# Optimization experiments

Measured on AMD Instinct MI355X. Metric: run time of the kernel, lower is better.

Reference implementation:

```python
import jax, jax.numpy as jnp
import numpy as np

B, C_IN, C_MID, C_OUT, H, W = 256, 2, 128, 64, 15, 15
N_RES = 4  # line_length//2 - 1 with line_length=11

# per-direction input offsets for kernel taps w0 and w2 (w1 is always center),
# matching fix_direction_order=True sparse 3x3 kernel construction:
# dir0 horizontal, dir1 vertical, dir2 anti-diagonal, dir3 main diagonal.
OFFSETS = (((0, -1), (0, 1)),
           ((-1, 0), (1, 0)),
           ((1, -1), (-1, 1)),
           ((-1, -1), (1, 1)))


def shift2d(x, di, dj):
    # out[..., i, j] = x[..., i+di, j+dj] with zero padding (di,dj in {-1,0,1})
    nd = x.ndim
    xp = jnp.pad(x, [(0, 0)] * (nd - 2) + [(1, 1), (1, 1)])
    h, w = x.shape[-2], x.shape[-1]
    return xp[..., 1 + di:1 + di + h, 1 + dj:1 + dj + w]


def dir_conv(x, w, b):
    # x: [4,B,Cin,H,W]; w: [Cout,Cin,3]; b: [Cout]
    x0 = jnp.stack([shift2d(x[d], *OFFSETS[d][0]) for d in range(4)])
    x2 = jnp.stack([shift2d(x[d], *OFFSETS[d][1]) for d in range(4)])
    y = (jnp.einsum('oc,dbchw->dbohw', w[..., 0], x0)
         + jnp.einsum('oc,dbchw->dbohw', w[..., 1], x)
         + jnp.einsum('oc,dbchw->dbohw', w[..., 2], x2))
    return y + b[None, None, :, None, None]


def conv1x1(x, w, b):
    # x: [4,B,Cin,H,W]; w: [Cout,Cin]; b: [Cout]
    return jnp.einsum('oc,dbchw->dbohw', w, x) + b[None, None, :, None, None]


def setup_inputs() -> dict:
    key = jax.random.key(0)
    ks = jax.random.split(key, 16)
    s_in = 1.0 / np.sqrt(3 * C_IN)
    s_mid = 1.0 / np.sqrt(3 * C_MID)
    s_pw = 1.0 / np.sqrt(C_MID)
    return {
        'x': jax.random.normal(ks[0], (B, C_IN, H, W), jnp.float32),
        'dconv0_w': jax.random.normal(ks[1], (C_MID, C_IN, 3), jnp.float32) * s_in,
        'dconv0_b': jnp.zeros((C_MID,), jnp.float32),
        'res_dconv_w': jax.random.normal(ks[2], (N_RES, C_MID, C_MID, 3), jnp.float32) * s_mid,
        'res_dconv_b': jnp.zeros((N_RES, C_MID), jnp.float32),
        'res_pw_w': jax.random.normal(ks[3], (N_RES, C_MID, C_MID), jnp.float32) * s_pw,
        'res_pw_b': jnp.zeros((N_RES, C_MID), jnp.float32),
        'c0_w1': jax.random.normal(ks[4], (C_MID, C_MID), jnp.float32) * s_pw,
        'c0_b1': jnp.zeros((C_MID,), jnp.float32),
        'c0_w2': jax.random.normal(ks[5], (C_MID, C_MID), jnp.float32) * s_pw,
        'c0_b2': jnp.zeros((C_MID,), jnp.float32),
        'final_w': jax.random.normal(ks[6], (C_OUT, C_MID), jnp.float32) * s_pw,
        'final_b': jnp.zeros((C_OUT,), jnp.float32),
    }


def reference(x, dconv0_w, dconv0_b, res_dconv_w, res_dconv_b,
              res_pw_w, res_pw_b, c0_w1, c0_b1, c0_w2, c0_b2,
              final_w, final_b):
    act = jax.nn.silu
    # all 4 direction streams start from the same input plane
    h = jnp.broadcast_to(x[None], (4,) + x.shape)  # [4,B,Cin,H,W]
    h = act(dir_conv(h, dconv0_w, dconv0_b))
    # DirectionalConvResBlocks (norm='none')
    for i in range(N_RES):
        r = h
        h = act(dir_conv(h, res_dconv_w[i], res_dconv_b[i]))
        h = act(conv1x1(h, res_pw_w[i], res_pw_b[i]))
        h = h + r
    # Conv0dResBlock (two 1x1 convs, middle_dim_multipler=1)
    r = h
    h = act(conv1x1(h, c0_w1, c0_b1))
    h = act(conv1x1(h, c0_w2, c0_b2))
    h = h + r
    # final 1x1 conv, then stack directions at dim=1 -> [B,4,Cout,H,W]
    h = conv1x1(h, final_w, final_b)
    return jnp.transpose(h, (1, 0, 2, 3, 4))
```

## Files before the change

### kernel.cpp

```cpp
#include <hip/hip_runtime.h>

using u16 = unsigned short;
using u32 = unsigned int;

typedef __bf16 bf16x8 __attribute__((ext_vector_type(8)));
typedef float  f32x4  __attribute__((ext_vector_type(4)));

#define NPOS   225
#define NT     15
#define ROWP   136
#define A_ROWS 289
#define B_ROWS 241
#define A_ELEMS (A_ROWS*ROWP)
#define B_ELEMS (B_ROWS*ROWP)
#define LDS_BYTES ((A_ELEMS + B_ELEMS)*2)
#define RSTRIDE17 (17*ROWP)

#define WA_PER_L 49152
#define WP_OFF   (4*WA_PER_L)
#define WP_PER   16384
#define WF_OFF   (WP_OFF + 6*WP_PER)
#define W_U16_TOTAL (WF_OFF + 8192)

__host__ __device__ __forceinline__ int permc(int c){
  return (c & ~0x3C) | (((c >> 2) & 3) << 4) | (((c >> 4) & 3) << 2);
}

__device__ __forceinline__ float bflo(u32 q){ return __uint_as_float(q << 16); }
__device__ __forceinline__ float bfhi(u32 q){ return __uint_as_float(q & 0xffff0000u); }
__device__ __forceinline__ u16 f2bf(float f){
  u32 u = __float_as_uint(f);
  return (u16)((u + 0x7fffu + ((u >> 16) & 1u)) >> 16);
}
__device__ __forceinline__ u32 packbf(float a, float b){
  union { __bf16 h[2]; u32 u; } r;
  r.h[0] = (__bf16)a; r.h[1] = (__bf16)b;
  return r.u;
}
__device__ __forceinline__ float silu_f(float x){
  return x * __builtin_amdgcn_rcpf(1.f + __expf(-x));
}
__device__ __forceinline__ f32x4 mfma16(bf16x8 a, bf16x8 b, f32x4 c){
  return __builtin_amdgcn_mfma_f32_16x16x32_bf16(a, b, c, 0, 0, 0);
}

__global__ void prep_w(const float* __restrict__ d0w, const float* __restrict__ d0b,
                       const float* __restrict__ rdw,
                       const float* __restrict__ rpw, const float* __restrict__ c1w,
                       const float* __restrict__ c2w, const float* __restrict__ fw,
                       float* __restrict__ ws)
{
  u16* wsb = (u16*)(ws + 896);
  const int total = 896 + W_U16_TOTAL;
  for (int idx = blockIdx.x*blockDim.x + threadIdx.x; idx < total; idx += gridDim.x*blockDim.x){
    if (idx < 768){
      int k = idx >> 7, s = idx & 127;
      ws[idx] = d0w[permc(s)*6 + k];
      continue;
    }
    if (idx < 896){
      int s = idx - 768;
      ws[idx] = d0b[permc(s)];
      continue;
    }
    int e = idx - 896;
    float v;
    if (e < WP_OFF){
      int L = e / WA_PER_L, r = e % WA_PER_L;
      int og = r / 24576; int r1 = r - og*24576;
      int tap = r1 >> 13; int r2 = r1 & 8191;
      int ot = r2 >> 11, kb = (r2 >> 9) & 3, l = (r2 >> 3) & 63, j = r2 & 7;
      int o = (og*4 + ot)*16 + (l & 15);
      int ks = kb*32 + ((l >> 4) << 3) + j;
      v = rdw[((L*128 + o)*128 + permc(ks))*3 + tap];
    } else if (e < WF_OFF){
      int t2 = e - WP_OFF;
      int i = t2 / WP_PER, r = t2 % WP_PER;
      int og2 = r >> 13;
      int ot = (r >> 11) & 3, kb = (r >> 9) & 3, l = (r >> 3) & 63, j = r & 7;
      int o = (og2*4 + ot)*16 + (l & 15);
      int ks = kb*32 + ((l >> 4) << 3) + j;
      v = (i < 4) ? rpw[(i*128 + o)*128 + permc(ks)]
        : (i == 4) ? c1w[o*128 + permc(ks)] : c2w[o*128 + permc(ks)];
    } else {
      int e2 = e - WF_OFF;
      int ot = e2 >> 11, kb = (e2 >> 9) & 3, l = (e2 >> 3) & 63, j = e2 & 7;
      int o = ot*16 + (l & 15);
      int ks = kb*32 + ((l >> 4) << 3) + j;
      v = fw[o*128 + permc(ks)];
    }
    wsb[e] = f2bf(v);
  }
}

__device__ __forceinline__ uint4 pack_silu2(const f32x4& a, const f32x4& b){
  uint4 q;
  q.x = packbf(silu_f(a[0]), silu_f(a[1]));
  q.y = packbf(silu_f(a[2]), silu_f(a[3]));
  q.z = packbf(silu_f(b[0]), silu_f(b[1]));
  q.w = packbf(silu_f(b[2]), silu_f(b[3]));
  return q;
}

template<int NTL>
__device__ __forceinline__ void dconv_mfma(const u16* __restrict__ As, u16* __restrict__ Bs,
    const u16* __restrict__ wloc, const float* __restrict__ bias,
    int lane, int og, int T0, int off0, int off2)
{
  const int col = lane & 15, kg = lane >> 4, koff = kg*8;
  f32x4 acc[4][NTL];
  #pragma unroll
  for (int ot=0; ot<4; ++ot){
    f32x4 bz = *(const f32x4*)(bias + og*64 + ot*16 + kg*4);
    #pragma unroll
    for (int t=0;t<NTL;++t) acc[ot][t] = bz;
  }
  const int c1 = (col+1)*ROWP + koff;
  #pragma unroll 1
  for (int tap=0; tap<3; ++tap){
    const int offr = (tap==0) ? off0 : (tap==1) ? 0 : off2;
    bf16x8 w[4][4];
    #pragma unroll
    for (int ot=0; ot<4; ++ot)
      #pragma unroll
      for (int kb=0; kb<4; ++kb)
        w[ot][kb] = *(const bf16x8*)(wloc + tap*8192 + ot*2048 + kb*512 + lane*8);
    #pragma unroll
    for (int t=0; t<NTL; ++t){
      const u16* s = As + (T0+t+1)*RSTRIDE17 + c1 + offr;
      __builtin_amdgcn_s_setprio(1);
      #pragma unroll
      for (int kb=0; kb<4; ++kb){
        bf16x8 v = *(const bf16x8*)(s + kb*32);
        acc[0][t] = mfma16(w[0][kb], v, acc[0][t]);
        acc[1][t] = mfma16(w[1][kb], v, acc[1][t]);
        acc[2][t] = mfma16(w[2][kb], v, acc[2][t]);
        acc[3][t] = mfma16(w[3][kb], v, acc[3][t]);
      }
      __builtin_amdgcn_s_setprio(0);
    }
  }
  if (col < 15){
    #pragma unroll
    for (int t=0;t<NTL;++t){
      u16* dp = Bs + ((T0+t)*16+col)*ROWP + og*64 + kg*16;
      uint4 q0 = pack_silu2(acc[0][t], acc[1][t]);
      uint4 q1 = pack_silu2(acc[2][t], acc[3][t]);
      *(uint4*)dp = q0;
      *(uint4*)(dp+8) = q1;
    }
  }
}

template<bool SRC_HALO, bool DST_HALO, bool RESID>
__device__ __forceinline__ void pw_mfma(const u16* __restrict__ src, u16* __restrict__ dst,
    const u16* __restrict__ wloc, const float* __restrict__ bias,
    int lane, int og2, int T0, int T1)
{
  const int col = lane & 15, kg = lane >> 4, koff = kg*8;
  bf16x8 wp[4][4];
  #pragma unroll
  for (int ot=0; ot<4; ++ot)
    #pragma unroll
    for (int kb=0; kb<4; ++kb)
      wp[ot][kb] = *(const bf16x8*)(wloc + og2*8192 + ot*2048 + kb*512 + lane*8);
  f32x4 bz[4];
  #pragma unroll
  for (int ot=0; ot<4; ++ot) bz[ot] = *(const f32x4*)(bias + og2*64 + ot*16 + kg*4);
  const int c1 = (col+1)*ROWP;
  #pragma unroll 2
  for (int tile=T0; tile<T1; ++tile){
    const int rh = (tile+1)*RSTRIDE17 + c1;
    const int rc = (tile*16+col)*ROWP;
    const u16* S = src + (SRC_HALO ? rh : rc) + koff;
    f32x4 a0 = bz[0], a1 = bz[1], a2 = bz[2], a3 = bz[3];
    __builtin_amdgcn_s_setprio(1);
    #pragma unroll
    for (int kb=0; kb<4; ++kb){
      bf16x8 v = *(const bf16x8*)(S + kb*32);
      a0 = mfma16(wp[0][kb], v, a0);
      a1 = mfma16(wp[1][kb], v, a1);
      a2 = mfma16(wp[2][kb], v, a2);
      a3 = mfma16(wp[3][kb], v, a3);
    }
    __builtin_amdgcn_s_setprio(0);
    if (col < 15){
      u16* dp = dst + (DST_HALO ? rh : rc) + og2*64 + kg*16;
      float s0 = silu_f(a0[0]), s1 = silu_f(a0[1]), s2 = silu_f(a0[2]), s3 = silu_f(a0[3]);
      float s4 = silu_f(a1[0]), s5 = silu_f(a1[1]), s6 = silu_f(a1[2]), s7 = silu_f(a1[3]);
      float s8 = silu_f(a2[0]), s9 = silu_f(a2[1]), sa = silu_f(a2[2]), sb = silu_f(a2[3]);
      float sc = silu_f(a3[0]), sd = silu_f(a3[1]), se = silu_f(a3[2]), sf = silu_f(a3[3]);
      if (RESID){
        uint4 r0 = *(const uint4*)dp;
        uint4 r1 = *(const uint4*)(dp+8);
        s0 += bflo(r0.x); s1 += bfhi(r0.x); s2 += bflo(r0.y); s3 += bfhi(r0.y);
        s4 += bflo(r0.z); s5 += bfhi(r0.z); s6 += bflo(r0.w); s7 += bfhi(r0.w);
        s8 += bflo(r1.x); s9 += bfhi(r1.x); sa += bflo(r1.y); sb += bfhi(r1.y);
        sc += bflo(r1.z); sd += bfhi(r1.z); se += bflo(r1.w); sf += bfhi(r1.w);
      }
      uint4 q0, q1;
      q0.x = packbf(s0, s1); q0.y = packbf(s2, s3);
      q0.z = packbf(s4, s5); q0.w = packbf(s6, s7);
      q1.x = packbf(s8, s9); q1.y = packbf(sa, sb);
      q1.z = packbf(sc, sd); q1.w = packbf(se, sf);
      *(uint4*)dp = q0;
      *(uint4*)(dp+8) = q1;
    }
  }
}

__device__ __forceinline__ void fin_mfma(const u16* __restrict__ As,
    const u16* __restrict__ wloc, const float* __restrict__ bias,
    float* __restrict__ out, int lane, int ogf, int T0, int T1, int bd)
{
  const int col = lane & 15, kg = lane >> 4, koff = kg*8;
  bf16x8 wf[2][4];
  #pragma unroll
  for (int ot=0; ot<2; ++ot)
    #pragma unroll
    for (int kb=0; kb<4; ++kb)
      wf[ot][kb] = *(const bf16x8*)(wloc + (ogf*2+ot)*2048 + kb*512 + lane*8);
  f32x4 bz0 = *(const f32x4*)(bias + ogf*32 + kg*4);
  f32x4 bz1 = *(const f32x4*)(bias + ogf*32 + 16 + kg*4);
  const int c1 = (col+1)*ROWP;
  #pragma unroll 1
  for (int tile=T0; tile<T1; ++tile){
    const u16* S = As + (tile+1)*RSTRIDE17 + c1 + koff;
    f32x4 a0 = bz0, a1 = bz1;
    __builtin_amdgcn_s_setprio(1);
    #pragma unroll
    for (int kb=0; kb<4; ++kb){
      bf16x8 v = *(const bf16x8*)(S + kb*32);
      a0 = mfma16(wf[0][kb], v, a0);
      a1 = mfma16(wf[1][kb], v, a1);
    }
    __builtin_amdgcn_s_setprio(0);
    if (col < 15){
      float* op = out + ((size_t)(bd*64 + ogf*32 + kg*4))*NPOS + tile*15 + col;
      op[0]      = a0[0];
      op[NPOS]   = a0[1];
      op[2*NPOS] = a0[2];
      op[3*NPOS] = a0[3];
      float* oq = op + 16*NPOS;
      oq[0]      = a1[0];
      oq[NPOS]   = a1[1];
      oq[2*NPOS] = a1[2];
      oq[3*NPOS] = a1[3];
    }
  }
}

__global__ void __launch_bounds__(512, 2)
mix9_main(const float* __restrict__ x,
          const float* __restrict__ b_rd,
          const float* __restrict__ b_rp,
          const float* __restrict__ b_c1,
          const float* __restrict__ b_c2,
          const float* __restrict__ b_fin,
          const float* __restrict__ wt,
          float* __restrict__ out)
{
  extern __shared__ u16 sm[];
  u16* As = sm;
  u16* Bs = sm + A_ELEMS;

  const int blk  = blockIdx.x;
  const int b    = blk >> 2, d = blk & 3;
  const int tid  = threadIdx.x;
  const int wave = __builtin_amdgcn_readfirstlane(tid >> 6);
  const int lane = tid & 63;

  const int ogd  = wave >> 2;
  const int pgd  = wave & 3;
  const int og2  = wave >> 2;
  const int ph4  = wave & 3;
  const int T0p  = ph4 * 4;
  const int T1p  = (ph4 == 3) ? NT : T0p + 4;
  const int ob   = wave * 16;

  const int DI0[4] = {0,-1, 1,-1}, DJ0[4] = {-1, 0,-1,-1};
  const int DI2[4] = {0, 1,-1, 1}, DJ2[4] = { 1, 0, 1, 1};
  const int di0 = DI0[d], dj0 = DJ0[d], di2 = DI2[d], dj2 = DJ2[d];
  const int off0 = (di0*17 + dj0)*ROWP;
  const int off2 = (di2*17 + dj2)*ROWP;

  for (int k2 = tid; k2 < A_ELEMS; k2 += 512) As[k2] = 0;
  float* xs = (float*)Bs;
  for (int k2 = tid; k2 < 2*NPOS; k2 += 512) xs[k2] = x[b*(2*NPOS) + k2];
  __syncthreads();

  const float* b0p = wt + 768;
  #pragma unroll 1
  for (int pb = 0; pb < 4; ++pb){
    int pp = pb*64 + lane;
    int i = pp >> 4, j = pp & 15;
    if (i >= 15 || j >= 15) continue;
    float acc[16];
    #pragma unroll
    for (int oo=0;oo<16;++oo) acc[oo] = b0p[ob+oo];
    #pragma unroll
    for (int c=0;c<2;++c){
      int i0=i+di0, j0=j+dj0, i2=i+di2, j2=j+dj2;
      float x0 = ((unsigned)i0<15u && (unsigned)j0<15u) ? xs[c*NPOS + i0*15 + j0] : 0.f;
      float x1 = xs[c*NPOS + i*15 + j];
      float x2 = ((unsigned)i2<15u && (unsigned)j2<15u) ? xs[c*NPOS + i2*15 + j2] : 0.f;
      const float* w0r = wt + (c*3+0)*128 + ob;
      const float* w1r = wt + (c*3+1)*128 + ob;
      const float* w2r = wt + (c*3+2)*128 + ob;
      #pragma unroll
      for (int oo=0;oo<16;++oo)
        acc[oo] = fmaf(w0r[oo],x0, fmaf(w1r[oo],x1, fmaf(w2r[oo],x2, acc[oo])));
    }
    u16* dp = As + ((i+1)*17 + (j+1))*ROWP + ob;
    #pragma unroll
    for (int oo=0;oo<16;oo+=2)
      *(u32*)(dp+oo) = packbf(silu_f(acc[oo]), silu_f(acc[oo+1]));
  }
  __syncthreads();

  const u16* wsb = (const u16*)(wt + 896);

  #pragma unroll 1
  for (int L = 0; L < 4; ++L){
    if (pgd == 3)
      dconv_mfma<3>(As, Bs, wsb + L*WA_PER_L + ogd*24576, b_rd + L*128, lane, ogd, 12, off0, off2);
    else
      dconv_mfma<4>(As, Bs, wsb + L*WA_PER_L + ogd*24576, b_rd + L*128, lane, ogd, pgd*4, off0, off2);
    __syncthreads();
    pw_mfma<false,true,true>(Bs, As, wsb + WP_OFF + L*WP_PER, b_rp + L*128, lane, og2, T0p, T1p);
    __syncthreads();
  }

  pw_mfma<true,false,false>(As, Bs, wsb + WP_OFF + 4*WP_PER, b_c1, lane, og2, T0p, T1p);
  __syncthreads();
  pw_mfma<false,true,true>(Bs, As, wsb + WP_OFF + 5*WP_PER, b_c2, lane, og2, T0p, T1p);
  __syncthreads();

  fin_mfma(As, wsb + WF_OFF, b_fin, out, lane, og2, T0p, T1p, b*4 + d);
}

extern "C" void kernel_launch(void* const* d_in, const int* in_sizes, int n_in,
                              void* d_out, int out_size, void* d_ws, size_t ws_size,
                              hipStream_t stream)
{
  const float* x     = (const float*)d_in[0];
  const float* w_d0  = (const float*)d_in[1];
  const float* b_d0  = (const float*)d_in[2];
  const float* w_rd  = (const float*)d_in[3];
  const float* b_rd  = (const float*)d_in[4];
  const float* w_rp  = (const float*)d_in[5];
  const float* b_rp  = (const float*)d_in[6];
  const float* w_c1  = (const float*)d_in[7];
  const float* b_c1  = (const float*)d_in[8];
  const float* w_c2  = (const float*)d_in[9];
  const float* b_c2  = (const float*)d_in[10];
  const float* w_fin = (const float*)d_in[11];
  const float* b_fin = (const float*)d_in[12];
  float* wt  = (float*)d_ws;
  float* out = (float*)d_out;

  prep_w<<<128, 512, 0, stream>>>(w_d0, b_d0, w_rd, w_rp, w_c1, w_c2, w_fin, wt);

  (void)hipFuncSetAttribute((const void*)mix9_main,
                            hipFuncAttributeMaxDynamicSharedMemorySize, LDS_BYTES);
  mix9_main<<<1024, 512, LDS_BYTES, stream>>>(x, b_rd, b_rp, b_c1, b_c2, b_fin, wt, out);
}
```

Before: 243.5 us.

## Switch matrix ops from 16x16x32 to 32x32x16 bf16 MFMA with new weight layout

Replaces the 16x16x32 MFMA tiling with 32x32x16 MFMA instructions across the directional conv, pointwise convs and final projection. Weights are re-laid out to match and channels are permuted with a new mapping. Each wave now covers 64 output channels over 64 spatial positions. The B buffer is padded to 256 rows so the tiles divide evenly. The aim is fewer instructions and LDS reads per FLOP, at the cost of some wasted compute on padding positions and larger accumulator register use.

After: 250.4 us. +2.9%, slower.

```diff
diff --git a/kernel.cpp b/kernel.cpp
--- a/kernel.cpp
+++ b/kernel.cpp
@@ -5,16 +5,15 @@
 
 typedef __bf16 bf16x8 __attribute__((ext_vector_type(8)));
 typedef float  f32x4  __attribute__((ext_vector_type(4)));
+typedef float  f32x16 __attribute__((ext_vector_type(16)));
 
 #define NPOS   225
-#define NT     15
 #define ROWP   136
 #define A_ROWS 289
-#define B_ROWS 241
+#define B_ROWS 256
 #define A_ELEMS (A_ROWS*ROWP)
 #define B_ELEMS (B_ROWS*ROWP)
 #define LDS_BYTES ((A_ELEMS + B_ELEMS)*2)
-#define RSTRIDE17 (17*ROWP)
 
 #define WA_PER_L 49152
 #define WP_OFF   (4*WA_PER_L)
@@ -22,8 +21,9 @@
 #define WF_OFF   (WP_OFF + 6*WP_PER)
 #define W_U16_TOTAL (WF_OFF + 8192)
 
-__host__ __device__ __forceinline__ int permc(int c){
-  return (c & ~0x3C) | (((c >> 2) & 3) << 4) | (((c >> 4) & 3) << 2);
+__host__ __device__ __forceinline__ int chof(int c){
+  int s = c & 31;
+  return (c & ~31) | (((s >> 4) & 1)*4 + ((s >> 2) & 3)*8 + (s & 3));
 }
 
 __device__ __forceinline__ float bflo(u32 q){ return __uint_as_float(q << 16); }
@@ -40,8 +40,30 @@
 __device__ __forceinline__ float silu_f(float x){
   return x * __builtin_amdgcn_rcpf(1.f + __expf(-x));
 }
-__device__ __forceinline__ f32x4 mfma16(bf16x8 a, bf16x8 b, f32x4 c){
-  return __builtin_amdgcn_mfma_f32_16x16x32_bf16(a, b, c, 0, 0, 0);
+__device__ __forceinline__ f32x16 mfma32(bf16x8 a, bf16x8 b, f32x16 c){
+  return __builtin_amdgcn_mfma_f32_32x32x16_bf16(a, b, c, 0, 0, 0);
+}
+
+__device__ __forceinline__ void pack16(const f32x16& a, uint4& lo, uint4& hi){
+  lo.x = packbf(silu_f(a[0]),  silu_f(a[1]));
+  lo.y = packbf(silu_f(a[2]),  silu_f(a[3]));
+  lo.z = packbf(silu_f(a[4]),  silu_f(a[5]));
+  lo.w = packbf(silu_f(a[6]),  silu_f(a[7]));
+  hi.x = packbf(silu_f(a[8]),  silu_f(a[9]));
+  hi.y = packbf(silu_f(a[10]), silu_f(a[11]));
+  hi.z = packbf(silu_f(a[12]), silu_f(a[13]));
+  hi.w = packbf(silu_f(a[14]), silu_f(a[15]));
+}
+__device__ __forceinline__ void pack16r(const f32x16& a, const uint4& r0, const uint4& r1,
+                                        uint4& lo, uint4& hi){
+  lo.x = packbf(silu_f(a[0])  + bflo(r0.x), silu_f(a[1])  + bfhi(r0.x));
+  lo.y = packbf(silu_f(a[2])  + bflo(r0.y), silu_f(a[3])  + bfhi(r0.y));
+  lo.z = packbf(silu_f(a[4])  + bflo(r0.z), silu_f(a[5])  + bfhi(r0.z));
+  lo.w = packbf(silu_f(a[6])  + bflo(r0.w), silu_f(a[7])  + bfhi(r0.w));
+  hi.x = packbf(silu_f(a[8])  + bflo(r1.x), silu_f(a[9])  + bfhi(r1.x));
+  hi.y = packbf(silu_f(a[10]) + bflo(r1.y), silu_f(a[11]) + bfhi(r1.y));
+  hi.z = packbf(silu_f(a[12]) + bflo(r1.z), silu_f(a[13]) + bfhi(r1.z));
+  hi.w = packbf(silu_f(a[14]) + bflo(r1.w), silu_f(a[15]) + bfhi(r1.w));
 }
 
 __global__ void prep_w(const float* __restrict__ d0w, const float* __restrict__ d0b,
@@ -55,197 +77,200 @@
   for (int idx = blockIdx.x*blockDim.x + threadIdx.x; idx < total; idx += gridDim.x*blockDim.x){
     if (idx < 768){
       int k = idx >> 7, s = idx & 127;
-      ws[idx] = d0w[permc(s)*6 + k];
+      ws[idx] = d0w[chof(s)*6 + k];
       continue;
     }
     if (idx < 896){
       int s = idx - 768;
-      ws[idx] = d0b[permc(s)];
+      ws[idx] = d0b[chof(s)];
       continue;
     }
     int e = idx - 896;
     float v;
     if (e < WP_OFF){
       int L = e / WA_PER_L, r = e % WA_PER_L;
-      int og = r / 24576; int r1 = r - og*24576;
-      int tap = r1 >> 13; int r2 = r1 & 8191;
-      int ot = r2 >> 11, kb = (r2 >> 9) & 3, l = (r2 >> 3) & 63, j = r2 & 7;
-      int o = (og*4 + ot)*16 + (l & 15);
-      int ks = kb*32 + ((l >> 4) << 3) + j;
-      v = rdw[((L*128 + o)*128 + permc(ks))*3 + tap];
+      int tap = r / 16384, r1 = r % 16384;
+      int m = r1 >> 11, r2 = r1 & 2047;
+      int ot = r2 >> 9, l = (r2 >> 3) & 63, j = r2 & 7;
+      int o = ot*32 + (l & 31);
+      int ck = chof(m*16 + ((l >> 5) << 3) + j);
+      v = rdw[((L*128 + o)*128 + ck)*3 + tap];
     } else if (e < WF_OFF){
       int t2 = e - WP_OFF;
       int i = t2 / WP_PER, r = t2 % WP_PER;
-      int og2 = r >> 13;
-      int ot = (r >> 11) & 3, kb = (r >> 9) & 3, l = (r >> 3) & 63, j = r & 7;
-      int o = (og2*4 + ot)*16 + (l & 15);
-      int ks = kb*32 + ((l >> 4) << 3) + j;
-      v = (i < 4) ? rpw[(i*128 + o)*128 + permc(ks)]
-        : (i == 4) ? c1w[o*128 + permc(ks)] : c2w[o*128 + permc(ks)];
+      int m = r >> 11, ot = (r >> 9) & 3, l = (r >> 3) & 63, j = r & 7;
+      int o = ot*32 + (l & 31);
+      int ck = chof(m*16 + ((l >> 5) << 3) + j);
+      v = (i < 4) ? rpw[(i*128 + o)*128 + ck]
+        : (i == 4) ? c1w[o*128 + ck] : c2w[o*128 + ck];
     } else {
       int e2 = e - WF_OFF;
-      int ot = e2 >> 11, kb = (e2 >> 9) & 3, l = (e2 >> 3) & 63, j = e2 & 7;
-      int o = ot*16 + (l & 15);
-      int ks = kb*32 + ((l >> 4) << 3) + j;
-      v = fw[o*128 + permc(ks)];
+      int m = e2 >> 10, ot = (e2 >> 9) & 1, l = (e2 >> 3) & 63, j = e2 & 7;
+      int o = ot*32 + (l & 31);
+      int ck = chof(m*16 + ((l >> 5) << 3) + j);
+      v = fw[o*128 + ck];
     }
     wsb[e] = f2bf(v);
   }
 }
 
-__device__ __forceinline__ uint4 pack_silu2(const f32x4& a, const f32x4& b){
-  uint4 q;
-  q.x = packbf(silu_f(a[0]), silu_f(a[1]));
-  q.y = packbf(silu_f(a[2]), silu_f(a[3]));
-  q.z = packbf(silu_f(b[0]), silu_f(b[1]));
-  q.w = packbf(silu_f(b[2]), silu_f(b[3]));
-  return q;
-}
-
-template<int NTL>
-__device__ __forceinline__ void dconv_mfma(const u16* __restrict__ As, u16* __restrict__ Bs,
-    const u16* __restrict__ wloc, const float* __restrict__ bias,
-    int lane, int og, int T0, int off0, int off2)
-{
-  const int col = lane & 15, kg = lane >> 4, koff = kg*8;
-  f32x4 acc[4][NTL];
-  #pragma unroll
-  for (int ot=0; ot<4; ++ot){
-    f32x4 bz = *(const f32x4*)(bias + og*64 + ot*16 + kg*4);
-    #pragma unroll
-    for (int t=0;t<NTL;++t) acc[ot][t] = bz;
-  }
-  const int c1 = (col+1)*ROWP + koff;
+__device__ __forceinline__ f32x16 bias16(const float* bb){
+  f32x16 bz;
+  #pragma unroll
+  for (int q=0;q<4;++q){
+    f32x4 b4 = *(const f32x4*)(bb + 8*q);
+    bz[4*q] = b4[0]; bz[4*q+1] = b4[1]; bz[4*q+2] = b4[2]; bz[4*q+3] = b4[3];
+  }
+  return bz;
+}
+
+__device__ __forceinline__ void dconv32(const u16* __restrict__ As, u16* __restrict__ Bs,
+    const u16* __restrict__ wl, const float* __restrict__ bias,
+    int lane, int og, int pg, int dr0, int dr2)
+{
+  const int p32 = lane & 31, h = lane >> 5;
+  f32x16 acc[2][2];
+  #pragma unroll
+  for (int o2=0;o2<2;++o2){
+    f32x16 bz = bias16(bias + (2*og+o2)*32 + 4*h);
+    acc[o2][0] = bz; acc[o2][1] = bz;
+  }
+  int base[2];
+  #pragma unroll
+  for (int t=0;t<2;++t){
+    int i = (pg*2+t)*2 + (p32 >> 4), j = p32 & 15;
+    base[t] = ((i+1)*17 + (j+1))*ROWP + h*8;
+  }
   #pragma unroll 1
   for (int tap=0; tap<3; ++tap){
-    const int offr = (tap==0) ? off0 : (tap==1) ? 0 : off2;
-    bf16x8 w[4][4];
-    #pragma unroll
-    for (int ot=0; ot<4; ++ot)
-      #pragma unroll
-      for (int kb=0; kb<4; ++kb)
-        w[ot][kb] = *(const bf16x8*)(wloc + tap*8192 + ot*2048 + kb*512 + lane*8);
-    #pragma unroll
-    for (int t=0; t<NTL; ++t){
-      const u16* s = As + (T0+t+1)*RSTRIDE17 + c1 + offr;
+    const int droff = ((tap==0) ? dr0 : (tap==1) ? 0 : dr2)*ROWP;
+    bf16x8 w0[8], w1[8];
+    #pragma unroll
+    for (int m=0;m<8;++m){
+      w0[m] = *(const bf16x8*)(wl + tap*16384 + m*2048 + (2*og  )*512 + lane*8);
+      w1[m] = *(const bf16x8*)(wl + tap*16384 + m*2048 + (2*og+1)*512 + lane*8);
+    }
+    #pragma unroll
+    for (int m=0;m<8;++m){
+      #pragma unroll
+      for (int t=0;t<2;++t){
+        bf16x8 v = *(const bf16x8*)(As + base[t] + droff + m*16);
+        __builtin_amdgcn_s_setprio(1);
+        acc[0][t] = mfma32(w0[m], v, acc[0][t]);
+        acc[1][t] = mfma32(w1[m], v, acc[1][t]);
+        __builtin_amdgcn_s_setprio(0);
+      }
+    }
+  }
+  #pragma unroll
+  for (int t=0;t<2;++t){
+    int pp = (pg*2+t)*32 + p32;
+    #pragma unroll
+    for (int o2=0;o2<2;++o2){
+      u16* dp = Bs + pp*ROWP + (2*og+o2)*32 + 16*h;
+      uint4 lo, hi; pack16(acc[o2][t], lo, hi);
+      *(uint4*)dp = lo; *(uint4*)(dp+8) = hi;
+    }
+  }
+}
+
+template<bool SRC_HALO, bool DST_HALO, bool RESID>
+__device__ __forceinline__ void pw32(const u16* __restrict__ src, u16* __restrict__ dst,
+    const u16* __restrict__ wl, const float* __restrict__ bias,
+    int lane, int og, int pg)
+{
+  const int p32 = lane & 31, h = lane >> 5;
+  f32x16 acc[2][2];
+  #pragma unroll
+  for (int o2=0;o2<2;++o2){
+    f32x16 bz = bias16(bias + (2*og+o2)*32 + 4*h);
+    acc[o2][0] = bz; acc[o2][1] = bz;
+  }
+  bf16x8 w0[8], w1[8];
+  #pragma unroll
+  for (int m=0;m<8;++m){
+    w0[m] = *(const bf16x8*)(wl + m*2048 + (2*og  )*512 + lane*8);
+    w1[m] = *(const bf16x8*)(wl + m*2048 + (2*og+1)*512 + lane*8);
+  }
+  int rsrc[2], rdst[2], valid[2];
+  #pragma unroll
+  for (int t=0;t<2;++t){
+    int i = (pg*2+t)*2 + (p32 >> 4), j = p32 & 15;
+    int r17 = ((i+1)*17 + (j+1))*ROWP;
+    int rc  = ((pg*2+t)*32 + p32)*ROWP;
+    rsrc[t] = SRC_HALO ? r17 : rc;
+    rdst[t] = DST_HALO ? r17 : rc;
+    valid[t] = (j < 15) && (i < 15);
+  }
+  #pragma unroll
+  for (int m=0;m<8;++m){
+    #pragma unroll
+    for (int t=0;t<2;++t){
+      bf16x8 v = *(const bf16x8*)(src + rsrc[t] + h*8 + m*16);
       __builtin_amdgcn_s_setprio(1);
-      #pragma unroll
-      for (int kb=0; kb<4; ++kb){
-        bf16x8 v = *(const bf16x8*)(s + kb*32);
-        acc[0][t] = mfma16(w[0][kb], v, acc[0][t]);
-        acc[1][t] = mfma16(w[1][kb], v, acc[1][t]);
-        acc[2][t] = mfma16(w[2][kb], v, acc[2][t]);
-        acc[3][t] = mfma16(w[3][kb], v, acc[3][t]);
+      acc[0][t] = mfma32(w0[m], v, acc[0][t]);
+      acc[1][t] = mfma32(w1[m], v, acc[1][t]);
+      __builtin_amdgcn_s_setprio(0);
+    }
+  }
+  #pragma unroll
+  for (int t=0;t<2;++t){
+    if (!DST_HALO || valid[t]){
+      #pragma unroll
+      for (int o2=0;o2<2;++o2){
+        u16* dp = dst + rdst[t] + (2*og+o2)*32 + 16*h;
+        uint4 lo, hi;
+        if (RESID){
+          uint4 r0 = *(const uint4*)dp;
+          uint4 r1 = *(const uint4*)(dp+8);
+          pack16r(acc[o2][t], r0, r1, lo, hi);
+        } else {
+          pack16(acc[o2][t], lo, hi);
+        }
+        *(uint4*)dp = lo; *(uint4*)(dp+8) = hi;
       }
+    }
+  }
+}
+
+__device__ __forceinline__ void fin32(const u16* __restrict__ As,
+    const u16* __restrict__ wl, const float* __restrict__ bias,
+    float* __restrict__ out, int lane, int og, int pg, int bd)
+{
+  const int p32 = lane & 31, h = lane >> 5;
+  f32x16 bz = bias16(bias + og*32 + 4*h);
+  f32x16 acc[2] = {bz, bz};
+  bf16x8 wf[8];
+  #pragma unroll
+  for (int m=0;m<8;++m)
+    wf[m] = *(const bf16x8*)(wl + m*1024 + og*512 + lane*8);
+  int base[2], ii[2], jj[2];
+  #pragma unroll
+  for (int t=0;t<2;++t){
+    ii[t] = (pg*2+t)*2 + (p32 >> 4); jj[t] = p32 & 15;
+    base[t] = ((ii[t]+1)*17 + (jj[t]+1))*ROWP + h*8;
+  }
+  #pragma unroll
+  for (int m=0;m<8;++m){
+    #pragma unroll
+    for (int t=0;t<2;++t){
+      bf16x8 v = *(const bf16x8*)(As + base[t] + m*16);
+      __builtin_amdgcn_s_setprio(1);
+      acc[t] = mfma32(wf[m], v, acc[t]);
       __builtin_amdgcn_s_setprio(0);
     }
   }
-  if (col < 15){
-    #pragma unroll
-    for (int t=0;t<NTL;++t){
-      u16* dp = Bs + ((T0+t)*16+col)*ROWP + og*64 + kg*16;
-      uint4 q0 = pack_silu2(acc[0][t], acc[1][t]);
-      uint4 q1 = pack_silu2(acc[2][t], acc[3][t]);
-      *(uint4*)dp = q0;
-      *(uint4*)(dp+8) = q1;
-    }
-  }
-}
-
-template<bool SRC_HALO, bool DST_HALO, bool RESID>
-__device__ __forceinline__ void pw_mfma(const u16* __restrict__ src, u16* __restrict__ dst,
-    const u16* __restrict__ wloc, const float* __restrict__ bias,
-    int lane, int og2, int T0, int T1)
-{
-  const int col = lane & 15, kg = lane >> 4, koff = kg*8;
-  bf16x8 wp[4][4];
-  #pragma unroll
-  for (int ot=0; ot<4; ++ot)
-    #pragma unroll
-    for (int kb=0; kb<4; ++kb)
-      wp[ot][kb] = *(const bf16x8*)(wloc + og2*8192 + ot*2048 + kb*512 + lane*8);
-  f32x4 bz[4];
-  #pragma unroll
-  for (int ot=0; ot<4; ++ot) bz[ot] = *(const f32x4*)(bias + og2*64 + ot*16 + kg*4);
-  const int c1 = (col+1)*ROWP;
-  #pragma unroll 2
-  for (int tile=T0; tile<T1; ++tile){
-    const int rh = (tile+1)*RSTRIDE17 + c1;
-    const int rc = (tile*16+col)*ROWP;
-    const u16* S = src + (SRC_HALO ? rh : rc) + koff;
-    f32x4 a0 = bz[0], a1 = bz[1], a2 = bz[2], a3 = bz[3];
-    __builtin_amdgcn_s_setprio(1);
-    #pragma unroll
-    for (int kb=0; kb<4; ++kb){
-      bf16x8 v = *(const bf16x8*)(S + kb*32);
-      a0 = mfma16(wp[0][kb], v, a0);
-      a1 = mfma16(wp[1][kb], v, a1);
-      a2 = mfma16(wp[2][kb], v, a2);
-      a3 = mfma16(wp[3][kb], v, a3);
-    }
-    __builtin_amdgcn_s_setprio(0);
-    if (col < 15){
-      u16* dp = dst + (DST_HALO ? rh : rc) + og2*64 + kg*16;
-      float s0 = silu_f(a0[0]), s1 = silu_f(a0[1]), s2 = silu_f(a0[2]), s3 = silu_f(a0[3]);
-      float s4 = silu_f(a1[0]), s5 = silu_f(a1[1]), s6 = silu_f(a1[2]), s7 = silu_f(a1[3]);
-      float s8 = silu_f(a2[0]), s9 = silu_f(a2[1]), sa = silu_f(a2[2]), sb = silu_f(a2[3]);
-      float sc = silu_f(a3[0]), sd = silu_f(a3[1]), se = silu_f(a3[2]), sf = silu_f(a3[3]);
-      if (RESID){
-        uint4 r0 = *(const uint4*)dp;
-        uint4 r1 = *(const uint4*)(dp+8);
-        s0 += bflo(r0.x); s1 += bfhi(r0.x); s2 += bflo(r0.y); s3 += bfhi(r0.y);
-        s4 += bflo(r0.z); s5 += bfhi(r0.z); s6 += bflo(r0.w); s7 += bfhi(r0.w);
-        s8 += bflo(r1.x); s9 += bfhi(r1.x); sa += bflo(r1.y); sb += bfhi(r1.y);
-        sc += bflo(r1.z); sd += bfhi(r1.z); se += bflo(r1.w); sf += bfhi(r1.w);
+  #pragma unroll
+  for (int t=0;t<2;++t){
+    if (jj[t] < 15 && ii[t] < 15){
+      #pragma unroll
+      for (int q=0;q<4;++q){
+        #pragma unroll
+        for (int r=0;r<4;++r){
+          int ch = og*32 + 4*h + 8*q + r;
+          out[((size_t)(bd*64 + ch))*NPOS + ii[t]*15 + jj[t]] = acc[t][4*q+r];
+        }
       }
-      uint4 q0, q1;
-      q0.x = packbf(s0, s1); q0.y = packbf(s2, s3);
-      q0.z = packbf(s4, s5); q0.w = packbf(s6, s7);
-      q1.x = packbf(s8, s9); q1.y = packbf(sa, sb);
-      q1.z = packbf(sc, sd); q1.w = packbf(se, sf);
-      *(uint4*)dp = q0;
-      *(uint4*)(dp+8) = q1;
-    }
-  }
-}
-
-__device__ __forceinline__ void fin_mfma(const u16* __restrict__ As,
-    const u16* __restrict__ wloc, const float* __restrict__ bias,
-    float* __restrict__ out, int lane, int ogf, int T0, int T1, int bd)
-{
-  const int col = lane & 15, kg = lane >> 4, koff = kg*8;
-  bf16x8 wf[2][4];
-  #pragma unroll
-  for (int ot=0; ot<2; ++ot)
-    #pragma unroll
-    for (int kb=0; kb<4; ++kb)
-      wf[ot][kb] = *(const bf16x8*)(wloc + (ogf*2+ot)*2048 + kb*512 + lane*8);
-  f32x4 bz0 = *(const f32x4*)(bias + ogf*32 + kg*4);
-  f32x4 bz1 = *(const f32x4*)(bias + ogf*32 + 16 + kg*4);
-  const int c1 = (col+1)*ROWP;
-  #pragma unroll 1
-  for (int tile=T0; tile<T1; ++tile){
-    const u16* S = As + (tile+1)*RSTRIDE17 + c1 + koff;
-    f32x4 a0 = bz0, a1 = bz1;
-    __builtin_amdgcn_s_setprio(1);
-    #pragma unroll
-    for (int kb=0; kb<4; ++kb){
-      bf16x8 v = *(const bf16x8*)(S + kb*32);
-      a0 = mfma16(wf[0][kb], v, a0);
-      a1 = mfma16(wf[1][kb], v, a1);
-    }
-    __builtin_amdgcn_s_setprio(0);
-    if (col < 15){
-      float* op = out + ((size_t)(bd*64 + ogf*32 + kg*4))*NPOS + tile*15 + col;
-      op[0]      = a0[0];
-      op[NPOS]   = a0[1];
-      op[2*NPOS] = a0[2];
-      op[3*NPOS] = a0[3];
-      float* oq = op + 16*NPOS;
-      oq[0]      = a1[0];
-      oq[NPOS]   = a1[1];
-      oq[2*NPOS] = a1[2];
-      oq[3*NPOS] = a1[3];
     }
   }
 }
@@ -269,52 +294,49 @@
   const int tid  = threadIdx.x;
   const int wave = __builtin_amdgcn_readfirstlane(tid >> 6);
   const int lane = tid & 63;
-
-  const int ogd  = wave >> 2;
-  const int pgd  = wave & 3;
-  const int og2  = wave >> 2;
-  const int ph4  = wave & 3;
-  const int T0p  = ph4 * 4;
-  const int T1p  = (ph4 == 3) ? NT : T0p + 4;
-  const int ob   = wave * 16;
+  const int og   = wave >> 2;
+  const int pg   = wave & 3;
 
   const int DI0[4] = {0,-1, 1,-1}, DJ0[4] = {-1, 0,-1,-1};
   const int DI2[4] = {0, 1,-1, 1}, DJ2[4] = { 1, 0, 1, 1};
   const int di0 = DI0[d], dj0 = DJ0[d], di2 = DI2[d], dj2 = DJ2[d];
-  const int off0 = (di0*17 + dj0)*ROWP;
-  const int off2 = (di2*17 + dj2)*ROWP;
+  const int dr0 = di0*17 + dj0;
+  const int dr2 = di2*17 + dj2;
 
   for (int k2 = tid; k2 < A_ELEMS; k2 += 512) As[k2] = 0;
   float* xs = (float*)Bs;
-  for (int k2 = tid; k2 < 2*NPOS; k2 += 512) xs[k2] = x[b*(2*NPOS) + k2];
+  if (tid < 450) xs[tid] = x[b*450 + tid];
   __syncthreads();
 
-  const float* b0p = wt + 768;
-  #pragma unroll 1
-  for (int pb = 0; pb < 4; ++pb){
-    int pp = pb*64 + lane;
-    int i = pp >> 4, j = pp & 15;
-    if (i >= 15 || j >= 15) continue;
-    float acc[16];
-    #pragma unroll
-    for (int oo=0;oo<16;++oo) acc[oo] = b0p[ob+oo];
-    #pragma unroll
-    for (int c=0;c<2;++c){
-      int i0=i+di0, j0=j+dj0, i2=i+di2, j2=j+dj2;
-      float x0 = ((unsigned)i0<15u && (unsigned)j0<15u) ? xs[c*NPOS + i0*15 + j0] : 0.f;
-      float x1 = xs[c*NPOS + i*15 + j];
-      float x2 = ((unsigned)i2<15u && (unsigned)j2<15u) ? xs[c*NPOS + i2*15 + j2] : 0.f;
-      const float* w0r = wt + (c*3+0)*128 + ob;
-      const float* w1r = wt + (c*3+1)*128 + ob;
-      const float* w2r = wt + (c*3+2)*128 + ob;
-      #pragma unroll
-      for (int oo=0;oo<16;++oo)
-        acc[oo] = fmaf(w0r[oo],x0, fmaf(w1r[oo],x1, fmaf(w2r[oo],x2, acc[oo])));
-    }
-    u16* dp = As + ((i+1)*17 + (j+1))*ROWP + ob;
-    #pragma unroll
-    for (int oo=0;oo<16;oo+=2)
-      *(u32*)(dp+oo) = packbf(silu_f(acc[oo]), silu_f(acc[oo+1]));
+  {
+    const float* b0p = wt + 768;
+    const int ob = wave * 16;
+    #pragma unroll 1
+    for (int pb = 0; pb < 4; ++pb){
+      int pp = pb*64 + lane;
+      int i = pp >> 4, j = pp & 15;
+      if (i >= 15 || j >= 15) continue;
+      float acc0[16];
+      #pragma unroll
+      for (int oo=0;oo<16;++oo) acc0[oo] = b0p[ob+oo];
+      #pragma unroll
+      for (int c=0;c<2;++c){
+        int i0=i+di0, j0=j+dj0, i2=i+di2, j2=j+dj2;
+        float x0 = ((unsigned)i0<15u && (unsigned)j0<15u) ? xs[c*NPOS + i0*15 + j0] : 0.f;
+        float x1 = xs[c*NPOS + i*15 + j];
+        float x2 = ((unsigned)i2<15u && (unsigned)j2<15u) ? xs[c*NPOS + i2*15 + j2] : 0.f;
+        const float* w0r = wt + (c*3+0)*128 + ob;
+        const float* w1r = wt + (c*3+1)*128 + ob;
+        const float* w2r = wt + (c*3+2)*128 + ob;
+        #pragma unroll
+        for (int oo=0;oo<16;++oo)
+          acc0[oo] = fmaf(w0r[oo],x0, fmaf(w1r[oo],x1, fmaf(w2r[oo],x2, acc0[oo])));
+      }
+      u16* dp = As + ((i+1)*17 + (j+1))*ROWP + ob;
+      #pragma unroll
+      for (int oo=0;oo<16;oo+=2)
+        *(u32*)(dp+oo) = packbf(silu_f(acc0[oo]), silu_f(acc0[oo+1]));
+    }
   }
   __syncthreads();
 
@@ -322,21 +344,18 @@
 
   #pragma unroll 1
   for (int L = 0; L < 4; ++L){
-    if (pgd == 3)
-      dconv_mfma<3>(As, Bs, wsb + L*WA_PER_L + ogd*24576, b_rd + L*128, lane, ogd, 12, off0, off2);
-    else
-      dconv_mfma<4>(As, Bs, wsb + L*WA_PER_L + ogd*24576, b_rd + L*128, lane, ogd, pgd*4, off0, off2);
+    dconv32(As, Bs, wsb + L*WA_PER_L, b_rd + L*128, lane, og, pg, dr0, dr2);
     __syncthreads();
-    pw_mfma<false,true,true>(Bs, As, wsb + WP_OFF + L*WP_PER, b_rp + L*128, lane, og2, T0p, T1p);
+    pw32<false,true,true>(Bs, As, wsb + WP_OFF + L*WP_PER, b_rp + L*128, lane, og, pg);
     __syncthreads();
   }
 
-  pw_mfma<true,false,false>(As, Bs, wsb + WP_OFF + 4*WP_PER, b_c1, lane, og2, T0p, T1p);
+  pw32<true,false,false>(As, Bs, wsb + WP_OFF + 4*WP_PER, b_c1, lane, og, pg);
   __syncthreads();
-  pw_mfma<false,true,true>(Bs, As, wsb + WP_OFF + 5*WP_PER, b_c2, lane, og2, T0p, T1p);
+  pw32<false,true,true>(Bs, As, wsb + WP_OFF + 5*WP_PER, b_c2, lane, og, pg);
   __syncthreads();
 
-  fin_mfma(As, wsb + WF_OFF, b_fin, out, lane, og2, T0p, T1p, b*4 + d);
+  fin32(As, wsb + WF_OFF, b_fin, out, lane, og, pg, b*4 + d);
 }
 
 extern "C" void kernel_launch(void* const* d_in, const int* in_sizes, int n_in,
```
